# Kernel tuning notes

Measured on AMD Instinct MI355X. Metric: run time of the kernel, lower is better.

Reference implementation:

```python
import jax, jax.numpy as jnp
import numpy as np

NUM_HEADS = 32  # head_dim = input_dim // num_heads = 32 == C (forced by matmul contraction)


def setup_inputs() -> dict:
    key = jax.random.key(0)
    ks = jax.random.split(key, 8)
    B, C, D3, H1 = 16, 32, 1, 32
    input_dim = 1024  # == C**2, forced by the final view(B, C, H1, W1)
    s = 0.02
    x1 = jax.random.normal(ks[0], (B, C, D3, H1, input_dim), jnp.float32)
    x2 = jax.random.normal(ks[1], (B, C, D3, H1, input_dim), jnp.float32)
    Wq = jax.random.normal(ks[2], (input_dim, input_dim), jnp.float32) * s
    bq = jax.random.normal(ks[3], (input_dim,), jnp.float32) * s
    Wk = jax.random.normal(ks[4], (input_dim, input_dim), jnp.float32) * s
    bk = jax.random.normal(ks[5], (input_dim,), jnp.float32) * s
    Wv = jax.random.normal(ks[6], (input_dim, input_dim), jnp.float32) * s
    bv = jax.random.normal(ks[7], (input_dim,), jnp.float32) * s
    return {"x1": x1, "x2": x2, "Wq": Wq, "bq": bq, "Wk": Wk, "bk": bk, "Wv": Wv, "bv": bv}


def reference(x1, x2, Wq, bq, Wk, bk, Wv, bv):
    B, C, _, H1, W1 = x1.shape  # W1 == input_dim (Linear acts on last dim)
    nh = NUM_HEADS
    hd = W1 // nh
    # Linear projections on the last axis (torch Linear: x @ W.T + b)
    q = (x1 @ Wq.T + bq).reshape(B, C, nh, hd, -1).transpose(0, 2, 4, 3, 1)  # (B, nh, L1, hd, C)
    k = (x2 @ Wk.T + bk).reshape(B, C, nh, hd, -1)                            # (B, C, nh, hd, L2)
    v = (x2 @ Wv.T + bv).reshape(B, C, nh, hd, -1)                            # (B, C, nh, hd, L2)
    # Broadcasted batched matmul: contracts q's trailing C axis with k's hd axis (C == hd).
    energy = jnp.matmul(q, k)                      # (B, C, L1, hd, L2)
    attention = jax.nn.softmax(energy, axis=-1)    # softmax over L2
    # Contracts v's L2 axis with attention's hd axis (L2 == hd).
    out = jnp.matmul(v, attention)                 # (B, C, L1, hd, L2)
    out = out.transpose(0, 2, 4, 3, 1).reshape(B, C, H1, W1)
    return out
```

## Files before the change

### kernel.cpp

```cpp
#include <hip/hip_runtime.h>
#include <cstdint>

typedef __bf16 bf16x8 __attribute__((ext_vector_type(8)));
typedef float f32x4 __attribute__((ext_vector_type(4)));
typedef unsigned short us8 __attribute__((ext_vector_type(8)));

__device__ __forceinline__ unsigned short f2bf(float f) {
  union { float f; uint32_t u; } c; c.f = f;
  uint32_t u = c.u + 0x7FFFu + ((c.u >> 16) & 1u);
  return (unsigned short)(u >> 16);
}

__global__ __launch_bounds__(256) void cvt5(
    const float* __restrict__ x1, const float* __restrict__ x2,
    const float* __restrict__ Wq, const float* __restrict__ Wk, const float* __restrict__ Wv,
    unsigned short* __restrict__ xb1, unsigned short* __restrict__ xb2,
    unsigned short* __restrict__ wb) {
  int z = blockIdx.y;
  const float* src; unsigned short* dst; int n4;
  if (z == 0)      { src = x1; dst = xb1;            n4 = 16777216 / 4; }
  else if (z == 1) { src = x2; dst = xb2;            n4 = 16777216 / 4; }
  else if (z == 2) { src = Wq; dst = wb;             n4 = 1048576 / 4; }
  else if (z == 3) { src = Wk; dst = wb + 1048576;   n4 = 1048576 / 4; }
  else             { src = Wv; dst = wb + 2*1048576; n4 = 1048576 / 4; }
  for (int i = blockIdx.x * 256 + threadIdx.x; i < n4; i += gridDim.x * 256) {
    float4 v = ((const float4*)src)[i];
    ushort4 o;
    o.x = f2bf(v.x); o.y = f2bf(v.y); o.z = f2bf(v.z); o.w = f2bf(v.w);
    ((ushort4*)dst)[i] = o;
  }
}

__global__ __launch_bounds__(256) void gemm_qkv(
    const unsigned short* __restrict__ xb1, const unsigned short* __restrict__ xb2,
    const unsigned short* __restrict__ wb,
    const float* __restrict__ bq, const float* __restrict__ bk, const float* __restrict__ bv,
    unsigned short* __restrict__ qkv) {
  __shared__ __attribute__((aligned(16))) unsigned short lA[128 * 32];
  __shared__ __attribute__((aligned(16))) unsigned short lB[128 * 32];
  const int z = blockIdx.z;
  const unsigned short* A = (z == 0) ? xb1 : xb2;
  const unsigned short* W = wb + z * 1048576;
  const float* bias = (z == 0) ? bq : (z == 1 ? bk : bv);
  unsigned short* C = qkv + z * 16777216;
  const int n0 = blockIdx.x * 128;
  const int m0 = blockIdx.y * 128;
  const int lane = threadIdx.x & 63;
  const int wv = threadIdx.x >> 6;
  const int wm = wv >> 1, wn = wv & 1;
  const int mr = lane & 15, quad = lane >> 4;

  f32x4 acc[4][4];
#pragma unroll
  for (int i = 0; i < 4; ++i)
#pragma unroll
    for (int j = 0; j < 4; ++j) acc[i][j] = (f32x4){0.f, 0.f, 0.f, 0.f};

  for (int k0 = 0; k0 < 1024; k0 += 32) {
#pragma unroll
    for (int c4 = 0; c4 < 4; ++c4) {
      int c = wv * 4 + c4;
      int isB = c >> 3;
      int cc = c & 7;
      int row = cc * 16 + (lane >> 2);
      const unsigned short* src = isB ? (W + (n0 + row) * 1024 + k0)
                                      : (A + (m0 + row) * 1024 + k0);
      const char* g = (const char*)src + (lane & 3) * 16;
      char* ldst = (char*)(isB ? lB : lA) + cc * 1024;
      __builtin_amdgcn_global_load_lds((const __attribute__((address_space(1))) void*)g,
                                       (__attribute__((address_space(3))) void*)ldst,
                                       16, 0, 0);
    }
    __syncthreads();
    bf16x8 af[4], bfr[4];
#pragma unroll
    for (int i = 0; i < 4; ++i)
      af[i] = *(const bf16x8*)(lA + (wm * 64 + i * 16 + mr) * 32 + quad * 8);
#pragma unroll
    for (int j = 0; j < 4; ++j)
      bfr[j] = *(const bf16x8*)(lB + (wn * 64 + j * 16 + mr) * 32 + quad * 8);
#pragma unroll
    for (int i = 0; i < 4; ++i)
#pragma unroll
      for (int j = 0; j < 4; ++j)
        acc[i][j] = __builtin_amdgcn_mfma_f32_16x16x32_bf16(af[i], bfr[j], acc[i][j], 0, 0, 0);
    __syncthreads();
  }
#pragma unroll
  for (int j = 0; j < 4; ++j) {
    int col = n0 + wn * 64 + j * 16 + mr;
    float bb = bias[col];
#pragma unroll
    for (int i = 0; i < 4; ++i) {
      int rbase = m0 + wm * 64 + i * 16 + quad * 4;
#pragma unroll
      for (int r = 0; r < 4; ++r)
        C[(rbase + r) * 1024 + col] = f2bf(acc[i][j][r] + bb);
    }
  }
}

__global__ __launch_bounds__(256) void attn(const unsigned short* __restrict__ qkv,
                                            float* __restrict__ obuf) {
  const unsigned short* qbuf = qkv;
  const unsigned short* kbuf = qkv + 16777216;
  const unsigned short* vbuf = qkv + 2 * 16777216;
  __shared__ __attribute__((aligned(16))) unsigned short qs[8192];
  __shared__ __attribute__((aligned(16))) unsigned short ks[4][1024];
  __shared__ __attribute__((aligned(16))) unsigned short vs[4][1024];
  __shared__ __attribute__((aligned(16))) unsigned short ats[4][1024];
  const int y0 = blockIdx.x * 8;
  const int x = blockIdx.y;
  const int b = blockIdx.z;
  const int lane = threadIdx.x & 63;
  const int wv = threadIdx.x >> 6;
  const int mr = lane & 15, quad = lane >> 4;

#pragma unroll
  for (int it = 0; it < 4; ++it) {
    int c = threadIdx.x + 256 * it;
    int t = c >> 5, m = c & 31;
    const uint4* src = (const uint4*)(qbuf + ((b * 1024 + t * 32 + x) * 1024 + m * 32 + y0));
    ((uint4*)qs)[c] = *src;
  }
  __syncthreads();

  for (int s = 0; s < 2; ++s) {
    int y = y0 + wv * 2 + s;
    int dy = wv * 2 + s;
    const unsigned short* krow = kbuf + ((b * 32 + x) * 32 + y) * 1024;
    const unsigned short* vrow = vbuf + ((b * 32 + x) * 32 + y) * 1024;
    ((uint4*)ks[wv])[lane] = ((const uint4*)krow)[lane];
    ((uint4*)ks[wv])[64 + lane] = ((const uint4*)krow)[64 + lane];
    ((uint4*)vs[wv])[lane] = ((const uint4*)vrow)[lane];
    ((uint4*)vs[wv])[64 + lane] = ((const uint4*)vrow)[64 + lane];
    __syncthreads();

    bf16x8 qa[2], kb[2];
#pragma unroll
    for (int mt = 0; mt < 2; ++mt) {
      us8 tmp;
#pragma unroll
      for (int j = 0; j < 8; ++j)
        tmp[j] = qs[((quad * 8 + j) * 32 + mt * 16 + mr) * 8 + dy];
      qa[mt] = __builtin_bit_cast(bf16x8, tmp);
    }
#pragma unroll
    for (int lt = 0; lt < 2; ++lt) {
      us8 tmp;
#pragma unroll
      for (int j = 0; j < 8; ++j)
        tmp[j] = ks[wv][(quad * 8 + j) * 32 + lt * 16 + mr];
      kb[lt] = __builtin_bit_cast(bf16x8, tmp);
    }
    f32x4 e[2][2];
#pragma unroll
    for (int mt = 0; mt < 2; ++mt)
#pragma unroll
      for (int lt = 0; lt < 2; ++lt) {
        f32x4 zz = (f32x4){0.f, 0.f, 0.f, 0.f};
        e[mt][lt] = __builtin_amdgcn_mfma_f32_16x16x32_bf16(qa[mt], kb[lt], zz, 0, 0, 0);
      }

#pragma unroll
    for (int mt = 0; mt < 2; ++mt)
#pragma unroll
      for (int r = 0; r < 4; ++r) {
        float v0 = e[mt][0][r], v1 = e[mt][1][r];
        float mx = fmaxf(v0, v1);
#pragma unroll
        for (int off = 1; off < 16; off <<= 1) mx = fmaxf(mx, __shfl_xor(mx, off));
        float p0 = __expf(v0 - mx), p1 = __expf(v1 - mx);
        float sm = p0 + p1;
#pragma unroll
        for (int off = 1; off < 16; off <<= 1) sm += __shfl_xor(sm, off);
        float inv = 1.0f / sm;
        p0 *= inv; p1 *= inv;
        int trow = mt * 16 + quad * 4 + r;
        ats[wv][trow * 32 + mr] = f2bf(p0);
        ats[wv][trow * 32 + 16 + mr] = f2bf(p1);
      }
    __syncthreads();

    bf16x8 va[2], pb[2];
#pragma unroll
    for (int i = 0; i < 2; ++i)
      va[i] = *(const bf16x8*)(&vs[wv][(i * 16 + mr) * 32 + quad * 8]);
#pragma unroll
    for (int lt = 0; lt < 2; ++lt) {
      us8 tmp;
#pragma unroll
      for (int j = 0; j < 8; ++j)
        tmp[j] = ats[wv][(quad * 8 + j) * 32 + lt * 16 + mr];
      pb[lt] = __builtin_bit_cast(bf16x8, tmp);
    }
    f32x4 o[2][2];
#pragma unroll
    for (int i = 0; i < 2; ++i)
#pragma unroll
      for (int lt = 0; lt < 2; ++lt) {
        f32x4 zz = (f32x4){0.f, 0.f, 0.f, 0.f};
        o[i][lt] = __builtin_amdgcn_mfma_f32_16x16x32_bf16(va[i], pb[lt], zz, 0, 0, 0);
      }

    float* orow = obuf + ((b * 32 + x) * 32 + y) * 1024;
#pragma unroll
    for (int i = 0; i < 2; ++i)
#pragma unroll
      for (int lt = 0; lt < 2; ++lt)
#pragma unroll
        for (int r = 0; r < 4; ++r)
          orow[(i * 16 + quad * 4 + r) * 32 + lt * 16 + mr] = o[i][lt][r];
    __syncthreads();
  }
}

__global__ __launch_bounds__(256) void transpose2(const float* __restrict__ obuf,
                                                  float* __restrict__ out) {
  __shared__ float t[32][33];
  const int m = blockIdx.x, y = blockIdx.y, b = blockIdx.z;
  int l = threadIdx.x & 31;
  int g = threadIdx.x >> 5;
  for (int xx = g; xx < 32; xx += 8)
    t[xx][l] = obuf[((b * 32 + xx) * 32 + y) * 1024 + m * 32 + l];
  __syncthreads();
  int xi = threadIdx.x & 31;
  for (int ll = g; ll < 32; ll += 8)
    out[((b * 32 + y) * 32 + ll) * 1024 + m * 32 + xi] = t[xi][ll];
}

extern "C" void kernel_launch(void* const* d_in, const int* in_sizes, int n_in,
                              void* d_out, int out_size, void* d_ws, size_t ws_size,
                              hipStream_t stream) {
  const float* x1 = (const float*)d_in[0];
  const float* x2 = (const float*)d_in[1];
  const float* Wq = (const float*)d_in[2];
  const float* bq = (const float*)d_in[3];
  const float* Wk = (const float*)d_in[4];
  const float* bk = (const float*)d_in[5];
  const float* Wv = (const float*)d_in[6];
  const float* bv = (const float*)d_in[7];
  float* out = (float*)d_out;

  char* ws = (char*)d_ws;
  unsigned short* xb1 = (unsigned short*)ws;
  unsigned short* xb2 = xb1 + 16777216;
  unsigned short* wb = xb2 + 16777216;
  unsigned short* qkv = wb + 3 * 1048576;
  float* obuf = (float*)ws;

  cvt5<<<dim3(2048, 5), 256, 0, stream>>>(x1, x2, Wq, Wk, Wv, xb1, xb2, wb);
  gemm_qkv<<<dim3(8, 128, 3), 256, 0, stream>>>(xb1, xb2, wb, bq, bk, bv, qkv);
  attn<<<dim3(4, 32, 16), 256, 0, stream>>>(qkv, obuf);
  transpose2<<<dim3(32, 32, 16), 256, 0, stream>>>(obuf, out);
}
```

Measured before the change: 390.0 us.

## Remap QKV GEMM blocks per XCD and drop per-wave attention barriers

The QKV GEMM now runs on a flat 1D grid. Block ids are decoded so that the eight N-tiles sharing one M row-block land on the same XCD, which lets them reuse the A tile through that XCD's L2 instead of refetching it from memory. The attention kernel also drops three __syncthreads per iteration. Each wave only touches its own ks/vs/ats LDS slices, so those block-wide barriers were not needed. The risk is that correctness now depends on in-wave LDS ordering and on the hardware's round-robin block-to-XCD dispatch assumption.

```diff
diff --git a/kernel.cpp b/kernel.cpp
--- a/kernel.cpp
+++ b/kernel.cpp
@@ -38,13 +38,19 @@
     unsigned short* __restrict__ qkv) {
   __shared__ __attribute__((aligned(16))) unsigned short lA[128 * 32];
   __shared__ __attribute__((aligned(16))) unsigned short lB[128 * 32];
-  const int z = blockIdx.z;
+  const int id = blockIdx.x;
+  const int xcd = id & 7;
+  const int j = id >> 3;
+  const int nb = j & 7;
+  const int g = j >> 3;
+  const int z = g >> 4;
+  const int mb = (g & 15) * 8 + xcd;
   const unsigned short* A = (z == 0) ? xb1 : xb2;
   const unsigned short* W = wb + z * 1048576;
   const float* bias = (z == 0) ? bq : (z == 1 ? bk : bv);
   unsigned short* C = qkv + z * 16777216;
-  const int n0 = blockIdx.x * 128;
-  const int m0 = blockIdx.y * 128;
+  const int n0 = nb * 128;
+  const int m0 = mb * 128;
   const int lane = threadIdx.x & 63;
   const int wv = threadIdx.x >> 6;
   const int wm = wv >> 1, wn = wv & 1;
@@ -54,7 +60,7 @@
 #pragma unroll
   for (int i = 0; i < 4; ++i)
 #pragma unroll
-    for (int j = 0; j < 4; ++j) acc[i][j] = (f32x4){0.f, 0.f, 0.f, 0.f};
+    for (int jj = 0; jj < 4; ++jj) acc[i][jj] = (f32x4){0.f, 0.f, 0.f, 0.f};
 
   for (int k0 = 0; k0 < 1024; k0 += 32) {
 #pragma unroll
@@ -65,9 +71,9 @@
       int row = cc * 16 + (lane >> 2);
       const unsigned short* src = isB ? (W + (n0 + row) * 1024 + k0)
                                       : (A + (m0 + row) * 1024 + k0);
-      const char* g = (const char*)src + (lane & 3) * 16;
+      const char* gp = (const char*)src + (lane & 3) * 16;
       char* ldst = (char*)(isB ? lB : lA) + cc * 1024;
-      __builtin_amdgcn_global_load_lds((const __attribute__((address_space(1))) void*)g,
+      __builtin_amdgcn_global_load_lds((const __attribute__((address_space(1))) void*)gp,
                                        (__attribute__((address_space(3))) void*)ldst,
                                        16, 0, 0);
     }
@@ -77,25 +83,25 @@
     for (int i = 0; i < 4; ++i)
       af[i] = *(const bf16x8*)(lA + (wm * 64 + i * 16 + mr) * 32 + quad * 8);
 #pragma unroll
-    for (int j = 0; j < 4; ++j)
-      bfr[j] = *(const bf16x8*)(lB + (wn * 64 + j * 16 + mr) * 32 + quad * 8);
+    for (int jj = 0; jj < 4; ++jj)
+      bfr[jj] = *(const bf16x8*)(lB + (wn * 64 + jj * 16 + mr) * 32 + quad * 8);
 #pragma unroll
     for (int i = 0; i < 4; ++i)
 #pragma unroll
-      for (int j = 0; j < 4; ++j)
-        acc[i][j] = __builtin_amdgcn_mfma_f32_16x16x32_bf16(af[i], bfr[j], acc[i][j], 0, 0, 0);
+      for (int jj = 0; jj < 4; ++jj)
+        acc[i][jj] = __builtin_amdgcn_mfma_f32_16x16x32_bf16(af[i], bfr[jj], acc[i][jj], 0, 0, 0);
     __syncthreads();
   }
 #pragma unroll
-  for (int j = 0; j < 4; ++j) {
-    int col = n0 + wn * 64 + j * 16 + mr;
+  for (int jj = 0; jj < 4; ++jj) {
+    int col = n0 + wn * 64 + jj * 16 + mr;
     float bb = bias[col];
 #pragma unroll
     for (int i = 0; i < 4; ++i) {
       int rbase = m0 + wm * 64 + i * 16 + quad * 4;
 #pragma unroll
       for (int r = 0; r < 4; ++r)
-        C[(rbase + r) * 1024 + col] = f2bf(acc[i][j][r] + bb);
+        C[(rbase + r) * 1024 + col] = f2bf(acc[i][jj][r] + bb);
     }
   }
 }
@@ -134,23 +140,22 @@
     ((uint4*)ks[wv])[64 + lane] = ((const uint4*)krow)[64 + lane];
     ((uint4*)vs[wv])[lane] = ((const uint4*)vrow)[lane];
     ((uint4*)vs[wv])[64 + lane] = ((const uint4*)vrow)[64 + lane];
-    __syncthreads();
 
     bf16x8 qa[2], kb[2];
 #pragma unroll
     for (int mt = 0; mt < 2; ++mt) {
       us8 tmp;
 #pragma unroll
-      for (int j = 0; j < 8; ++j)
-        tmp[j] = qs[((quad * 8 + j) * 32 + mt * 16 + mr) * 8 + dy];
+      for (int jj = 0; jj < 8; ++jj)
+        tmp[jj] = qs[((quad * 8 + jj) * 32 + mt * 16 + mr) * 8 + dy];
       qa[mt] = __builtin_bit_cast(bf16x8, tmp);
     }
 #pragma unroll
     for (int lt = 0; lt < 2; ++lt) {
       us8 tmp;
 #pragma unroll
-      for (int j = 0; j < 8; ++j)
-        tmp[j] = ks[wv][(quad * 8 + j) * 32 + lt * 16 + mr];
+      for (int jj = 0; jj < 8; ++jj)
+        tmp[jj] = ks[wv][(quad * 8 + jj) * 32 + lt * 16 + mr];
       kb[lt] = __builtin_bit_cast(bf16x8, tmp);
     }
     f32x4 e[2][2];
@@ -180,7 +185,6 @@
         ats[wv][trow * 32 + mr] = f2bf(p0);
         ats[wv][trow * 32 + 16 + mr] = f2bf(p1);
       }
-    __syncthreads();
 
     bf16x8 va[2], pb[2];
 #pragma unroll
@@ -190,8 +194,8 @@
     for (int lt = 0; lt < 2; ++lt) {
       us8 tmp;
 #pragma unroll
-      for (int j = 0; j < 8; ++j)
-        tmp[j] = ats[wv][(quad * 8 + j) * 32 + lt * 16 + mr];
+      for (int jj = 0; jj < 8; ++jj)
+        tmp[jj] = ats[wv][(quad * 8 + jj) * 32 + lt * 16 + mr];
       pb[lt] = __builtin_bit_cast(bf16x8, tmp);
     }
     f32x4 o[2][2];
@@ -211,7 +215,6 @@
 #pragma unroll
         for (int r = 0; r < 4; ++r)
           orow[(i * 16 + quad * 4 + r) * 32 + lt * 16 + mr] = o[i][lt][r];
-    __syncthreads();
   }
 }
 
@@ -250,7 +253,7 @@
   float* obuf = (float*)ws;
 
   cvt5<<<dim3(2048, 5), 256, 0, stream>>>(x1, x2, Wq, Wk, Wv, xb1, xb2, wb);
-  gemm_qkv<<<dim3(8, 128, 3), 256, 0, stream>>>(xb1, xb2, wb, bq, bk, bv, qkv);
+  gemm_qkv<<<dim3(3072), 256, 0, stream>>>(xb1, xb2, wb, bq, bk, bv, qkv);
   attn<<<dim3(4, 32, 16), 256, 0, stream>>>(qkv, obuf);
   transpose2<<<dim3(32, 32, 16), 256, 0, stream>>>(obuf, out);
 }
```

After: 366.2 us. -6.1%, faster.
